# Performance work log

Hardware: AMD Instinct MI355X
Metric: run time of the kernel (lower is better)

## Reference

```python
import jax, jax.numpy as jnp
import numpy as np

N = 300000   # total atoms
E = 600000   # directed edges
G = 8192     # molecules in batch
D = 6        # node_feat_dim
H = 128      # hidden_dim
OUT = 256    # embedding_dim
L = 4        # num GIN layers


def setup_inputs() -> dict:
    key = jax.random.key(0)
    ks = jax.random.split(key, 12)
    s_in = 1.0 / np.sqrt(D)
    s_h = 1.0 / np.sqrt(H)
    return {
        "x": jax.random.normal(ks[0], (N, D), jnp.float32),
        "edge_index": jax.random.randint(ks[1], (2, E), 0, N, dtype=jnp.int32),
        "batch": jnp.sort(jax.random.randint(ks[2], (N,), 0, G, dtype=jnp.int32)),
        "W_enc": jax.random.normal(ks[3], (D, H), jnp.float32) * s_in,
        "b_enc": jnp.zeros((H,), jnp.float32),
        "W1": jax.random.normal(ks[4], (L, H, H), jnp.float32) * s_h,
        "b1": jnp.zeros((L, H), jnp.float32),
        "W2": jax.random.normal(ks[5], (L, H, H), jnp.float32) * s_h,
        "b2": jnp.zeros((L, H), jnp.float32),
        "W_out": jax.random.normal(ks[6], (H, OUT), jnp.float32) * s_h,
        "b_out": jnp.zeros((OUT,), jnp.float32),
    }


def reference(x, edge_index, batch, W_enc, b_enc, W1, b1, W2, b2, W_out, b_out):
    n = x.shape[0]
    src, dst = edge_index[0], edge_index[1]
    # node encoder
    h = x @ W_enc + b_enc                                   # [N, H]
    # stacked GINConv: out = mlp((1+eps)*x + sum_neighbors), eps = 0
    for l in range(L):
        agg = jax.ops.segment_sum(h[src], dst, num_segments=n)  # gather + scatter-add
        z = h + agg
        z = jax.nn.relu(z @ W1[l] + b1[l]) @ W2[l] + b2[l]      # GIN MLP
        h = jax.nn.relu(z)                                       # outer F.relu
    # global mean pool over graphs
    sums = jax.ops.segment_sum(h, batch, num_segments=G)        # [G, H]
    counts = jax.ops.segment_sum(jnp.ones((n, 1), h.dtype), batch, num_segments=G)
    pooled = sums / jnp.maximum(counts, 1.0)
    return pooled @ W_out + b_out                                # [G, OUT]
```

## Files before the change

kernel.cpp:

```cpp
#include <hip/hip_runtime.h>

#define HD 128

typedef unsigned short ushort_t;
typedef __attribute__((ext_vector_type(8))) unsigned short us8;
typedef __attribute__((ext_vector_type(8))) short s8b;
typedef __attribute__((ext_vector_type(16))) float f32x16;

__device__ __forceinline__ float b2f(unsigned short u) {
    union { unsigned int i; float f; } v; v.i = ((unsigned int)u) << 16; return v.f;
}
__device__ __forceinline__ unsigned short f2b(float f) {
    union { float f; unsigned int i; } v; v.f = f;
    unsigned int u = v.i;
    return (unsigned short)((u + 0x7fffu + ((u >> 16) & 1u)) >> 16);
}
__device__ __forceinline__ unsigned int pk2(float a, float b) {
    return (unsigned int)f2b(a) | ((unsigned int)f2b(b) << 16);
}

__device__ __forceinline__ void load8f(const float* p, float* o) {
    float4 a = *reinterpret_cast<const float4*>(p);
    float4 b = *reinterpret_cast<const float4*>(p + 4);
    o[0]=a.x;o[1]=a.y;o[2]=a.z;o[3]=a.w;o[4]=b.x;o[5]=b.y;o[6]=b.z;o[7]=b.w;
}
__device__ __forceinline__ void store8b(ushort_t* p, const float* s) {
    us8 v;
#pragma unroll
    for (int j = 0; j < 8; ++j) v[j] = f2b(s[j]);
    *reinterpret_cast<us8*>(p) = v;
}

__device__ __forceinline__ void store1(float* p, float v) { *p = v; }
__device__ __forceinline__ void store1(ushort_t* p, float v) { *p = f2b(v); }

__device__ __forceinline__ int lowerb(const int* __restrict__ a, int n, int v) {
    int lo = 0, hi = n;
    while (lo < hi) { int m = (lo + hi) >> 1; if (a[m] < v) lo = m + 1; else hi = m; }
    return lo;
}

__global__ void hist_kernel(const int* __restrict__ dst, int* __restrict__ deg, int e) {
    int i = blockIdx.x * blockDim.x + threadIdx.x;
    if (i < e) atomicAdd(&deg[dst[i]], 1);
}

#define SCAN_NT 256
#define SCAN_BPT 8
#define SCAN_CHUNK (SCAN_NT * SCAN_BPT)

__global__ __launch_bounds__(SCAN_NT) void scan_a(const int* __restrict__ deg,
                                                  int* __restrict__ bsum, int n) {
    int tid = threadIdx.x;
    int base = blockIdx.x * SCAN_CHUNK + tid * SCAN_BPT;
    int sum = 0;
    if (base + SCAN_BPT <= n) {
        int4 v0 = *reinterpret_cast<const int4*>(deg + base);
        int4 v1 = *reinterpret_cast<const int4*>(deg + base + 4);
        sum = v0.x + v0.y + v0.z + v0.w + v1.x + v1.y + v1.z + v1.w;
    } else {
        for (int j = 0; j < SCAN_BPT; ++j) { int i = base + j; if (i < n) sum += deg[i]; }
    }
    __shared__ int sd[SCAN_NT];
    sd[tid] = sum; __syncthreads();
    for (int off = SCAN_NT / 2; off > 0; off >>= 1) {
        if (tid < off) sd[tid] += sd[tid + off];
        __syncthreads();
    }
    if (tid == 0) bsum[blockIdx.x] = sd[0];
}

__global__ __launch_bounds__(1024) void scan_b(int* __restrict__ bsum, int nb) {
    __shared__ int ps[1024];
    int tid = threadIdx.x;
    int v = (tid < nb) ? bsum[tid] : 0;
    ps[tid] = v; __syncthreads();
    for (int off = 1; off < 1024; off <<= 1) {
        int t = (tid >= off) ? ps[tid - off] : 0;
        __syncthreads();
        ps[tid] += t;
        __syncthreads();
    }
    if (tid < nb) bsum[tid] = ps[tid] - v;
}

__global__ __launch_bounds__(SCAN_NT) void scan_c(const int* __restrict__ deg,
                                                  const int* __restrict__ bsum,
                                                  int* __restrict__ rowptr,
                                                  int* __restrict__ cursor,
                                                  int n, int etot) {
    int tid = threadIdx.x;
    int base = blockIdx.x * SCAN_CHUNK + tid * SCAN_BPT;
    int vals[SCAN_BPT];
    if (base + SCAN_BPT <= n) {
        int4 v0 = *reinterpret_cast<const int4*>(deg + base);
        int4 v1 = *reinterpret_cast<const int4*>(deg + base + 4);
        vals[0]=v0.x; vals[1]=v0.y; vals[2]=v0.z; vals[3]=v0.w;
        vals[4]=v1.x; vals[5]=v1.y; vals[6]=v1.z; vals[7]=v1.w;
    } else {
        for (int j = 0; j < SCAN_BPT; ++j) { int i = base + j; vals[j] = (i < n) ? deg[i] : 0; }
    }
    int sum = 0;
#pragma unroll
    for (int j = 0; j < SCAN_BPT; ++j) sum += vals[j];
    __shared__ int ps[SCAN_NT];
    ps[tid] = sum; __syncthreads();
    for (int off = 1; off < SCAN_NT; off <<= 1) {
        int t = (tid >= off) ? ps[tid - off] : 0;
        __syncthreads();
        ps[tid] += t;
        __syncthreads();
    }
    int run = bsum[blockIdx.x] + ps[tid] - sum;
#pragma unroll
    for (int j = 0; j < SCAN_BPT; ++j) {
        int i = base + j;
        if (i < n) { rowptr[i] = run; cursor[i] = run; run += vals[j]; }
    }
    if (blockIdx.x == 0 && tid == 0) rowptr[n] = etot;
}

__global__ void fill_kernel(const int* __restrict__ src, const int* __restrict__ dst,
                            int* __restrict__ cursor, int* __restrict__ col, int e) {
    int i = blockIdx.x * blockDim.x + threadIdx.x;
    if (i < e) { int slot = atomicAdd(&cursor[dst[i]], 1); col[slot] = src[i]; }
}

__global__ void pack_kernel(const float* __restrict__ W, ushort_t* __restrict__ Wp,
                            int nmat, int ld, int mat_stride, int col_off) {
    int idx = blockIdx.x * blockDim.x + threadIdx.x;
    if (idx >= nmat * 2048) return;
    int lane = idx & 63;
    int ks = (idx >> 6) & 7;
    int j = (idx >> 9) & 3;
    int mat = idx >> 11;
    const float* Wm = W + (size_t)mat * mat_stride;
    int k0 = ks * 16 + (lane >> 5) * 8;
    int n = mat * col_off + j * 32 + (lane & 31);
    us8 o;
#pragma unroll
    for (int e = 0; e < 8; ++e) o[e] = f2b(Wm[(size_t)(k0 + e) * ld + n]);
    *reinterpret_cast<us8*>(Wp + (size_t)idx * 8) = o;
}

__global__ void xagg_kernel(const float* __restrict__ x, const int* __restrict__ rowptr,
                            const int* __restrict__ col, float* __restrict__ xa, int n) {
    int node = blockIdx.x * blockDim.x + threadIdx.x;
    if (node >= n) return;
    const float2* xr = reinterpret_cast<const float2*>(x + (size_t)node * 6);
    float2 a0 = xr[0], a1 = xr[1], a2 = xr[2];
    int lo = rowptr[node], hi = rowptr[node + 1];
    for (int i = lo; i < hi; ++i) {
        const float2* xs = reinterpret_cast<const float2*>(x + (size_t)col[i] * 6);
        float2 s0 = xs[0], s1 = xs[1], s2 = xs[2];
        a0.x += s0.x; a0.y += s0.y; a1.x += s1.x; a1.y += s1.y; a2.x += s2.x; a2.y += s2.y;
    }
    float cnt = (float)(1 + hi - lo);
    float4 o0; o0.x = a0.x; o0.y = a0.y; o0.z = a1.x; o0.w = a1.y;
    float4 o1; o1.x = a2.x; o1.y = a2.y; o1.z = cnt; o1.w = 0.f;
    reinterpret_cast<float4*>(xa + (size_t)node * 8)[0] = o0;
    reinterpret_cast<float4*>(xa + (size_t)node * 8)[1] = o1;
}

__global__ void enc2_kernel(const float* __restrict__ xa, const float* __restrict__ W,
                            const float* __restrict__ b, ushort_t* __restrict__ z, int n) {
    int t = blockIdx.x * blockDim.x + threadIdx.x;
    int q = t >> 4, g = t & 15;
    int node0 = q * 4;
    if (node0 >= n) return;
    float w[6][8];
#pragma unroll
    for (int d = 0; d < 6; ++d) load8f(W + d * HD + g * 8, w[d]);
    float bias[8];
    load8f(b + g * 8, bias);
#pragma unroll
    for (int u = 0; u < 4; ++u) {
        int node = node0 + u;
        if (node >= n) break;
        float4 a0 = reinterpret_cast<const float4*>(xa + (size_t)node * 8)[0];
        float4 a1 = reinterpret_cast<const float4*>(xa + (size_t)node * 8)[1];
        float xv[6] = {a0.x, a0.y, a0.z, a0.w, a1.x, a1.y};
        float cnt = a1.z;
        float acc[8];
#pragma unroll
        for (int j = 0; j < 8; ++j) acc[j] = cnt * bias[j];
#pragma unroll
        for (int d = 0; d < 6; ++d)
#pragma unroll
            for (int j = 0; j < 8; ++j) acc[j] += xv[d] * w[d][j];
        store8b(z + (size_t)node * HD + g * 8, acc);
    }
}

__device__ __forceinline__ void gemm1_repack(const s8b* __restrict__ sW, const s8b* bz,
                                             const float* __restrict__ b1,
                                             int lane, int h, s8b* a2) {
#pragma unroll
    for (int j = 0; j < 4; ++j) {
        f32x16 c;
#pragma unroll
        for (int i = 0; i < 16; ++i) c[i] = 0.f;
#pragma unroll
        for (int ks = 0; ks < 8; ++ks)
            c = __builtin_amdgcn_mfma_f32_32x32x16_bf16(sW[(j * 8 + ks) * 64 + lane], bz[ks], c, 0, 0, 0);
        {
            float4 bv0 = *reinterpret_cast<const float4*>(b1 + j * 32 + 0  + 4 * h);
            float4 bv1 = *reinterpret_cast<const float4*>(b1 + j * 32 + 8  + 4 * h);
            unsigned int w00 = pk2(fmaxf(c[0] + bv0.x, 0.f), fmaxf(c[1] + bv0.y, 0.f));
            unsigned int w01 = pk2(fmaxf(c[2] + bv0.z, 0.f), fmaxf(c[3] + bv0.w, 0.f));
            unsigned int w10 = pk2(fmaxf(c[4] + bv1.x, 0.f), fmaxf(c[5] + bv1.y, 0.f));
            unsigned int w11 = pk2(fmaxf(c[6] + bv1.z, 0.f), fmaxf(c[7] + bv1.w, 0.f));
            unsigned int p00 = (unsigned int)__shfl_xor((int)w00, 32);
            unsigned int p01 = (unsigned int)__shfl_xor((int)w01, 32);
            unsigned int p10 = (unsigned int)__shfl_xor((int)w10, 32);
            unsigned int p11 = (unsigned int)__shfl_xor((int)w11, 32);
            union { unsigned int u[4]; s8b v; } t;
            t.u[0] = h ? p10 : w00;
            t.u[1] = h ? p11 : w01;
            t.u[2] = h ? w10 : p00;
            t.u[3] = h ? w11 : p01;
            a2[2 * j] = t.v;
        }
        {
            float4 bv2 = *reinterpret_cast<const float4*>(b1 + j * 32 + 16 + 4 * h);
            float4 bv3 = *reinterpret_cast<const float4*>(b1 + j * 32 + 24 + 4 * h);
            unsigned int w20 = pk2(fmaxf(c[8]  + bv2.x, 0.f), fmaxf(c[9]  + bv2.y, 0.f));
            unsigned int w21 = pk2(fmaxf(c[10] + bv2.z, 0.f), fmaxf(c[11] + bv2.w, 0.f));
            unsigned int w30 = pk2(fmaxf(c[12] + bv3.x, 0.f), fmaxf(c[13] + bv3.y, 0.f));
            unsigned int w31 = pk2(fmaxf(c[14] + bv3.z, 0.f), fmaxf(c[15] + bv3.w, 0.f));
            unsigned int p20 = (unsigned int)__shfl_xor((int)w20, 32);
            unsigned int p21 = (unsigned int)__shfl_xor((int)w21, 32);
            unsigned int p30 = (unsigned int)__shfl_xor((int)w30, 32);
            unsigned int p31 = (unsigned int)__shfl_xor((int)w31, 32);
            union { unsigned int u[4]; s8b v; } t;
            t.u[0] = h ? p30 : w20;
            t.u[1] = h ? p31 : w21;
            t.u[2] = h ? w30 : p20;
            t.u[3] = h ? w31 : p21;
            a2[2 * j + 1] = t.v;
        }
    }
}

__device__ __forceinline__ void gemm2_store(const s8b* __restrict__ sW, const s8b* a2,
                                            const float* __restrict__ b2,
                                            int lane, int h, int row0,
                                            ushort_t* __restrict__ out) {
    const int r32 = lane & 31;
#pragma unroll
    for (int j = 0; j < 4; ++j) {
        f32x16 c;
#pragma unroll
        for (int i = 0; i < 16; ++i) c[i] = 0.f;
#pragma unroll
        for (int ks = 0; ks < 8; ++ks)
            c = __builtin_amdgcn_mfma_f32_32x32x16_bf16(a2[ks], sW[(j * 8 + ks) * 64 + lane], c, 0, 0, 0);
        const int ccol = j * 32 + r32;
        const float bv = b2[ccol];
        const int rbase = row0 + 4 * h;
#pragma unroll
        for (int reg = 0; reg < 16; ++reg) {
            int row = rbase + (reg & 3) + 8 * (reg >> 2);
            out[(size_t)row * HD + ccol] = f2b(fmaxf(c[reg] + bv, 0.f));
        }
    }
}

__global__ __launch_bounds__(1024, 4) void mlp_fused(
    ushort_t* __restrict__ z,
    const ushort_t* __restrict__ Wp1, const ushort_t* __restrict__ Wp2,
    const float* __restrict__ b1, const float* __restrict__ b2)
{
    __shared__ s8b sW1[2048];
    __shared__ s8b sW2[2048];

    const int tid = threadIdx.x;
    for (int i = tid; i < 2048; i += 1024) {
        sW1[i] = reinterpret_cast<const s8b*>(Wp1)[i];
        sW2[i] = reinterpret_cast<const s8b*>(Wp2)[i];
    }
    __syncthreads();

    const int lane = tid & 63;
    const int r32  = lane & 31;
    const int h    = lane >> 5;
    const int row0 = blockIdx.x * 512 + (tid >> 6) * 32;
    const int arow = row0 + r32;
    const int koff = h * 8;

    s8b bz[8];
#pragma unroll
    for (int ks = 0; ks < 8; ++ks)
        bz[ks] = *reinterpret_cast<const s8b*>(z + (size_t)arow * HD + ks * 16 + koff);

    s8b a2[8];
    gemm1_repack(sW1, bz, b1, lane, h, a2);
    gemm2_store(sW2, a2, b2, lane, h, row0, z);
}

__global__ __launch_bounds__(1024, 4) void gin_layer(
    const ushort_t* __restrict__ hin, const int* __restrict__ rowptr,
    const int* __restrict__ col,
    const ushort_t* __restrict__ Wp1, const ushort_t* __restrict__ Wp2,
    const float* __restrict__ b1, const float* __restrict__ b2,
    ushort_t* __restrict__ hout, int n)
{
    __shared__ s8b sW1[2048];
    __shared__ s8b sW2[2048];

    const int tid = threadIdx.x;
    for (int i = tid; i < 2048; i += 1024) {
        sW1[i] = reinterpret_cast<const s8b*>(Wp1)[i];
        sW2[i] = reinterpret_cast<const s8b*>(Wp2)[i];
    }
    __syncthreads();

    const int lane = tid & 63;
    const int r32  = lane & 31;
    const int h    = lane >> 5;
    const int row0 = blockIdx.x * 512 + (tid >> 6) * 32;
    const int arow = row0 + r32;
    const int koff = h * 8;

    const bool valid = (arow < n);
    const int lo = valid ? rowptr[arow] : 0;
    const int hi = valid ? rowptr[arow + 1] : 0;
    const ushort_t* hbase = hin + (size_t)arow * HD + koff;

    s8b bz[8];

    {
        float facc[4][8];
        if (valid) {
#pragma unroll
            for (int q = 0; q < 4; ++q) {
                us8 v = *reinterpret_cast<const us8*>(hbase + q * 16);
#pragma unroll
                for (int e = 0; e < 8; ++e) facc[q][e] = b2f(v[e]);
            }
            for (int i = lo; i < hi; ++i) {
                const ushort_t* hs = hin + (size_t)col[i] * HD + koff;
#pragma unroll
                for (int q = 0; q < 4; ++q) {
                    us8 v = *reinterpret_cast<const us8*>(hs + q * 16);
#pragma unroll
                    for (int e = 0; e < 8; ++e) facc[q][e] += b2f(v[e]);
                }
            }
        } else {
#pragma unroll
            for (int q = 0; q < 4; ++q)
#pragma unroll
                for (int e = 0; e < 8; ++e) facc[q][e] = 0.f;
        }
#pragma unroll
        for (int q = 0; q < 4; ++q)
#pragma unroll
            for (int e = 0; e < 8; ++e) bz[q][e] = (short)f2b(facc[q][e]);
    }

    {
        float facc[4][8];
        if (valid) {
#pragma unroll
            for (int q = 0; q < 4; ++q) {
                us8 v = *reinterpret_cast<const us8*>(hbase + 64 + q * 16);
#pragma unroll
                for (int e = 0; e < 8; ++e) facc[q][e] = b2f(v[e]);
            }
            for (int i = lo; i < hi; ++i) {
                const ushort_t* hs = hin + (size_t)col[i] * HD + koff + 64;
#pragma unroll
                for (int q = 0; q < 4; ++q) {
                    us8 v = *reinterpret_cast<const us8*>(hs + q * 16);
#pragma unroll
                    for (int e = 0; e < 8; ++e) facc[q][e] += b2f(v[e]);
                }
            }
        } else {
#pragma unroll
            for (int q = 0; q < 4; ++q)
#pragma unroll
                for (int e = 0; e < 8; ++e) facc[q][e] = 0.f;
        }
#pragma unroll
        for (int q = 0; q < 4; ++q)
#pragma unroll
            for (int e = 0; e < 8; ++e) bz[4 + q][e] = (short)f2b(facc[q][e]);
    }

    s8b a2[8];
    gemm1_repack(sW1, bz, b1, lane, h, a2);
    gemm2_store(sW2, a2, b2, lane, h, row0, hout);
}

template<typename TO, bool RELU>
__global__ __launch_bounds__(256) void gemm_mfma(
    const ushort_t* __restrict__ A, const ushort_t* __restrict__ Wp,
    const float* __restrict__ bias, TO* __restrict__ out, int ldo)
{
    __shared__ s8b sW[2048];
    const int tid = threadIdx.x;
    for (int i = tid; i < 2048; i += 256)
        sW[i] = reinterpret_cast<const s8b*>(Wp)[i];
    __syncthreads();

    const int lane = tid & 63;
    const int row0 = blockIdx.x * 128 + (tid >> 6) * 32;
    const int arow = row0 + (lane & 31);
    const int koff = (lane >> 5) * 8;

    s8b a[8];
#pragma unroll
    for (int ks = 0; ks < 8; ++ks)
        a[ks] = *reinterpret_cast<const s8b*>(A + (size_t)arow * HD + ks * 16 + koff);

#pragma unroll
    for (int j = 0; j < 4; ++j) {
        f32x16 acc;
#pragma unroll
        for (int i = 0; i < 16; ++i) acc[i] = 0.f;
#pragma unroll
        for (int ks = 0; ks < 8; ++ks)
            acc = __builtin_amdgcn_mfma_f32_32x32x16_bf16(a[ks], sW[(j * 8 + ks) * 64 + lane], acc, 0, 0, 0);
        const int col = j * 32 + (lane & 31);
        const float bv = bias[col];
        const int rbase = row0 + 4 * (lane >> 5);
#pragma unroll
        for (int reg = 0; reg < 16; ++reg) {
            int row = rbase + (reg & 3) + 8 * (reg >> 2);
            float v = acc[reg] + bv;
            if (RELU) v = fmaxf(v, 0.f);
            store1(out + (size_t)row * ldo + col, v);
        }
    }
}

__global__ __launch_bounds__(128) void pool_kernel(const ushort_t* __restrict__ h,
                                                   const int* __restrict__ batch,
                                                   ushort_t* __restrict__ pooled, int n) {
    int g = blockIdx.x;
    int c = threadIdx.x;
    int start = lowerb(batch, n, g);
    int end = lowerb(batch, n, g + 1);
    float s = 0.f;
    for (int i = start; i < end; ++i) s += b2f(h[(size_t)i * HD + c]);
    int cnt = end - start; if (cnt < 1) cnt = 1;
    pooled[(size_t)g * HD + c] = f2b(s / (float)cnt);
}

extern "C" void kernel_launch(void* const* d_in, const int* in_sizes, int n_in,
                              void* d_out, int out_size, void* d_ws, size_t ws_size,
                              hipStream_t stream) {
    const float* x      = (const float*)d_in[0];
    const int*   edge   = (const int*)d_in[1];
    const int*   batch  = (const int*)d_in[2];
    const float* W_enc  = (const float*)d_in[3];
    const float* b_enc  = (const float*)d_in[4];
    const float* W1     = (const float*)d_in[5];
    const float* b1     = (const float*)d_in[6];
    const float* W2     = (const float*)d_in[7];
    const float* b2     = (const float*)d_in[8];
    const float* W_out  = (const float*)d_in[9];
    const float* b_out  = (const float*)d_in[10];

    const int N = in_sizes[0] / 6;
    const int E = in_sizes[1] / 2;
    const int G = out_size / 256;
    const int L = in_sizes[5] / (HD * HD);
    const int Npad = ((N + 511) / 512) * 512;

    const int* srcv = edge;
    const int* dstv = edge + E;

    size_t off = 0;
    auto alloc = [&](size_t bytes) -> char* {
        char* p = (char*)d_ws + off;
        off += (bytes + 255) & ~(size_t)255;
        return p;
    };
    ushort_t* bufA   = (ushort_t*)alloc((size_t)Npad * HD * 2);
    ushort_t* bufB   = (ushort_t*)alloc((size_t)Npad * HD * 2);
    ushort_t* pooled = (ushort_t*)alloc((size_t)G * HD * 2);
    ushort_t* Wp1    = (ushort_t*)alloc((size_t)L * 16384 * 2);
    ushort_t* Wp2    = (ushort_t*)alloc((size_t)L * 16384 * 2);
    ushort_t* WpO    = (ushort_t*)alloc((size_t)2 * 16384 * 2);
    float* xaggb = (float*)alloc((size_t)N * 8 * 4);
    int* rowptr = (int*)alloc((size_t)(N + 1) * 4);
    int* cursor = (int*)alloc((size_t)N * 4);
    int* colidx = (int*)alloc((size_t)E * 4);
    int* deg    = (int*)alloc((size_t)N * 4);
    int* bsum   = (int*)alloc((size_t)1024 * 4);
    (void)ws_size;

    const int nb = (N + SCAN_CHUNK - 1) / SCAN_CHUNK;
    hipMemsetAsync(deg, 0, (size_t)N * 4, stream);
    hist_kernel<<<(E + 255) / 256, 256, 0, stream>>>(dstv, deg, E);
    scan_a<<<nb, SCAN_NT, 0, stream>>>(deg, bsum, N);
    scan_b<<<1, 1024, 0, stream>>>(bsum, nb);
    scan_c<<<nb, SCAN_NT, 0, stream>>>(deg, bsum, rowptr, cursor, N, E);
    fill_kernel<<<(E + 255) / 256, 256, 0, stream>>>(srcv, dstv, cursor, colidx, E);

    pack_kernel<<<(L * 2048 + 255) / 256, 256, 0, stream>>>(W1, Wp1, L, HD, HD * HD, 0);
    pack_kernel<<<(L * 2048 + 255) / 256, 256, 0, stream>>>(W2, Wp2, L, HD, HD * HD, 0);
    pack_kernel<<<(2 * 2048 + 255) / 256, 256, 0, stream>>>(W_out, WpO, 2, 256, 0, 128);

    xagg_kernel<<<(N + 255) / 256, 256, 0, stream>>>(x, rowptr, colidx, xaggb, N);
    {
        int threads = ((N + 3) / 4) * 16;
        enc2_kernel<<<(threads + 255) / 256, 256, 0, stream>>>(xaggb, W_enc, b_enc, bufA, N);
    }
    const int nblk = Npad / 512;
    mlp_fused<<<nblk, 1024, 0, stream>>>(bufA, Wp1, Wp2, b1, b2);

    ushort_t* cur = bufA;
    ushort_t* oth = bufB;
    for (int l = 1; l < L; ++l) {
        gin_layer<<<nblk, 1024, 0, stream>>>(
            cur, rowptr, colidx,
            Wp1 + (size_t)l * 16384, Wp2 + (size_t)l * 16384,
            b1 + (size_t)l * HD, b2 + (size_t)l * HD, oth, N);
        ushort_t* t = cur; cur = oth; oth = t;
    }

    pool_kernel<<<G, 128, 0, stream>>>(cur, batch, pooled, N);

    float* outp = (float*)d_out;
    gemm_mfma<float, false><<<G / 128, 256, 0, stream>>>(pooled, WpO, b_out, outp, 256);
    gemm_mfma<float, false><<<G / 128, 256, 0, stream>>>(pooled, WpO + 16384, b_out + 128, outp + 128, 256);
}
```

Measured before the change: 463.4 us.

## Use persistent blocks with atomic work-stealing over 32-row tiles in GIN kernels

The fused MLP and GIN layer kernels now launch a fixed grid of 512 blocks instead of one block per 512 rows. Each wavefront repeatedly grabs a 32-row tile from a global atomic counter until all tiles are done. This spreads the uneven per-row gather cost across waves and loads the shared weights once per persistent block rather than once per tile group. In exchange it adds one atomic per tile and a memset for the counters, and the grid size is now fixed.

```diff
diff --git a/kernel.cpp b/kernel.cpp
--- a/kernel.cpp
+++ b/kernel.cpp
@@ -269,7 +269,8 @@
 __global__ __launch_bounds__(1024, 4) void mlp_fused(
     ushort_t* __restrict__ z,
     const ushort_t* __restrict__ Wp1, const ushort_t* __restrict__ Wp2,
-    const float* __restrict__ b1, const float* __restrict__ b2)
+    const float* __restrict__ b1, const float* __restrict__ b2,
+    int ntiles, int* __restrict__ counter)
 {
     __shared__ s8b sW1[2048];
     __shared__ s8b sW2[2048];
@@ -284,18 +285,25 @@
     const int lane = tid & 63;
     const int r32  = lane & 31;
     const int h    = lane >> 5;
-    const int row0 = blockIdx.x * 512 + (tid >> 6) * 32;
-    const int arow = row0 + r32;
     const int koff = h * 8;
 
-    s8b bz[8];
-#pragma unroll
-    for (int ks = 0; ks < 8; ++ks)
-        bz[ks] = *reinterpret_cast<const s8b*>(z + (size_t)arow * HD + ks * 16 + koff);
-
-    s8b a2[8];
-    gemm1_repack(sW1, bz, b1, lane, h, a2);
-    gemm2_store(sW2, a2, b2, lane, h, row0, z);
+    while (true) {
+        int t = 0;
+        if (lane == 0) t = atomicAdd(counter, 1);
+        t = __shfl(t, 0);
+        if (t >= ntiles) break;
+        const int row0 = t * 32;
+        const int arow = row0 + r32;
+
+        s8b bz[8];
+#pragma unroll
+        for (int ks = 0; ks < 8; ++ks)
+            bz[ks] = *reinterpret_cast<const s8b*>(z + (size_t)arow * HD + ks * 16 + koff);
+
+        s8b a2[8];
+        gemm1_repack(sW1, bz, b1, lane, h, a2);
+        gemm2_store(sW2, a2, b2, lane, h, row0, z);
+    }
 }
 
 __global__ __launch_bounds__(1024, 4) void gin_layer(
@@ -303,7 +311,7 @@
     const int* __restrict__ col,
     const ushort_t* __restrict__ Wp1, const ushort_t* __restrict__ Wp2,
     const float* __restrict__ b1, const float* __restrict__ b2,
-    ushort_t* __restrict__ hout, int n)
+    ushort_t* __restrict__ hout, int n, int ntiles, int* __restrict__ counter)
 {
     __shared__ s8b sW1[2048];
     __shared__ s8b sW2[2048];
@@ -318,80 +326,87 @@
     const int lane = tid & 63;
     const int r32  = lane & 31;
     const int h    = lane >> 5;
-    const int row0 = blockIdx.x * 512 + (tid >> 6) * 32;
-    const int arow = row0 + r32;
     const int koff = h * 8;
 
-    const bool valid = (arow < n);
-    const int lo = valid ? rowptr[arow] : 0;
-    const int hi = valid ? rowptr[arow + 1] : 0;
-    const ushort_t* hbase = hin + (size_t)arow * HD + koff;
-
-    s8b bz[8];
-
-    {
-        float facc[4][8];
-        if (valid) {
-#pragma unroll
-            for (int q = 0; q < 4; ++q) {
-                us8 v = *reinterpret_cast<const us8*>(hbase + q * 16);
-#pragma unroll
-                for (int e = 0; e < 8; ++e) facc[q][e] = b2f(v[e]);
+    while (true) {
+        int t = 0;
+        if (lane == 0) t = atomicAdd(counter, 1);
+        t = __shfl(t, 0);
+        if (t >= ntiles) break;
+        const int row0 = t * 32;
+        const int arow = row0 + r32;
+
+        const bool valid = (arow < n);
+        const int lo = valid ? rowptr[arow] : 0;
+        const int hi = valid ? rowptr[arow + 1] : 0;
+        const ushort_t* hbase = hin + (size_t)arow * HD + koff;
+
+        s8b bz[8];
+
+        {
+            float facc[4][8];
+            if (valid) {
+#pragma unroll
+                for (int q = 0; q < 4; ++q) {
+                    us8 v = *reinterpret_cast<const us8*>(hbase + q * 16);
+#pragma unroll
+                    for (int e = 0; e < 8; ++e) facc[q][e] = b2f(v[e]);
+                }
+                for (int i = lo; i < hi; ++i) {
+                    const ushort_t* hs = hin + (size_t)col[i] * HD + koff;
+#pragma unroll
+                    for (int q = 0; q < 4; ++q) {
+                        us8 v = *reinterpret_cast<const us8*>(hs + q * 16);
+#pragma unroll
+                        for (int e = 0; e < 8; ++e) facc[q][e] += b2f(v[e]);
+                    }
+                }
+            } else {
+#pragma unroll
+                for (int q = 0; q < 4; ++q)
+#pragma unroll
+                    for (int e = 0; e < 8; ++e) facc[q][e] = 0.f;
             }
-            for (int i = lo; i < hi; ++i) {
-                const ushort_t* hs = hin + (size_t)col[i] * HD + koff;
+#pragma unroll
+            for (int q = 0; q < 4; ++q)
+#pragma unroll
+                for (int e = 0; e < 8; ++e) bz[q][e] = (short)f2b(facc[q][e]);
+        }
+
+        {
+            float facc[4][8];
+            if (valid) {
 #pragma unroll
                 for (int q = 0; q < 4; ++q) {
-                    us8 v = *reinterpret_cast<const us8*>(hs + q * 16);
-#pragma unroll
-                    for (int e = 0; e < 8; ++e) facc[q][e] += b2f(v[e]);
+                    us8 v = *reinterpret_cast<const us8*>(hbase + 64 + q * 16);
+#pragma unroll
+                    for (int e = 0; e < 8; ++e) facc[q][e] = b2f(v[e]);
                 }
+                for (int i = lo; i < hi; ++i) {
+                    const ushort_t* hs = hin + (size_t)col[i] * HD + koff + 64;
+#pragma unroll
+                    for (int q = 0; q < 4; ++q) {
+                        us8 v = *reinterpret_cast<const us8*>(hs + q * 16);
+#pragma unroll
+                        for (int e = 0; e < 8; ++e) facc[q][e] += b2f(v[e]);
+                    }
+                }
+            } else {
+#pragma unroll
+                for (int q = 0; q < 4; ++q)
+#pragma unroll
+                    for (int e = 0; e < 8; ++e) facc[q][e] = 0.f;
             }
-        } else {
 #pragma unroll
             for (int q = 0; q < 4; ++q)
 #pragma unroll
-                for (int e = 0; e < 8; ++e) facc[q][e] = 0.f;
+                for (int e = 0; e < 8; ++e) bz[4 + q][e] = (short)f2b(facc[q][e]);
         }
-#pragma unroll
-        for (int q = 0; q < 4; ++q)
-#pragma unroll
-            for (int e = 0; e < 8; ++e) bz[q][e] = (short)f2b(facc[q][e]);
-    }
-
-    {
-        float facc[4][8];
-        if (valid) {
-#pragma unroll
-            for (int q = 0; q < 4; ++q) {
-                us8 v = *reinterpret_cast<const us8*>(hbase + 64 + q * 16);
-#pragma unroll
-                for (int e = 0; e < 8; ++e) facc[q][e] = b2f(v[e]);
-            }
-            for (int i = lo; i < hi; ++i) {
-                const ushort_t* hs = hin + (size_t)col[i] * HD + koff + 64;
-#pragma unroll
-                for (int q = 0; q < 4; ++q) {
-                    us8 v = *reinterpret_cast<const us8*>(hs + q * 16);
-#pragma unroll
-                    for (int e = 0; e < 8; ++e) facc[q][e] += b2f(v[e]);
-                }
-            }
-        } else {
-#pragma unroll
-            for (int q = 0; q < 4; ++q)
-#pragma unroll
-                for (int e = 0; e < 8; ++e) facc[q][e] = 0.f;
-        }
-#pragma unroll
-        for (int q = 0; q < 4; ++q)
-#pragma unroll
-            for (int e = 0; e < 8; ++e) bz[4 + q][e] = (short)f2b(facc[q][e]);
-    }
-
-    s8b a2[8];
-    gemm1_repack(sW1, bz, b1, lane, h, a2);
-    gemm2_store(sW2, a2, b2, lane, h, row0, hout);
+
+        s8b a2[8];
+        gemm1_repack(sW1, bz, b1, lane, h, a2);
+        gemm2_store(sW2, a2, b2, lane, h, row0, hout);
+    }
 }
 
 template<typename TO, bool RELU>
@@ -469,6 +484,7 @@
     const int G = out_size / 256;
     const int L = in_sizes[5] / (HD * HD);
     const int Npad = ((N + 511) / 512) * 512;
+    const int ntiles = (N + 31) / 32;
 
     const int* srcv = edge;
     const int* dstv = edge + E;
@@ -491,7 +507,10 @@
     int* colidx = (int*)alloc((size_t)E * 4);
     int* deg    = (int*)alloc((size_t)N * 4);
     int* bsum   = (int*)alloc((size_t)1024 * 4);
+    int* counters = (int*)alloc((size_t)16 * 4);
     (void)ws_size;
+
+    hipMemsetAsync(counters, 0, 16 * 4, stream);
 
     const int nb = (N + SCAN_CHUNK - 1) / SCAN_CHUNK;
     hipMemsetAsync(deg, 0, (size_t)N * 4, stream);
@@ -510,16 +529,16 @@
         int threads = ((N + 3) / 4) * 16;
         enc2_kernel<<<(threads + 255) / 256, 256, 0, stream>>>(xaggb, W_enc, b_enc, bufA, N);
     }
-    const int nblk = Npad / 512;
-    mlp_fused<<<nblk, 1024, 0, stream>>>(bufA, Wp1, Wp2, b1, b2);
+    const int PBLK = 512;
+    mlp_fused<<<PBLK, 1024, 0, stream>>>(bufA, Wp1, Wp2, b1, b2, ntiles, counters + 0);
 
     ushort_t* cur = bufA;
     ushort_t* oth = bufB;
     for (int l = 1; l < L; ++l) {
-        gin_layer<<<nblk, 1024, 0, stream>>>(
+        gin_layer<<<PBLK, 1024, 0, stream>>>(
             cur, rowptr, colidx,
             Wp1 + (size_t)l * 16384, Wp2 + (size_t)l * 16384,
-            b1 + (size_t)l * HD, b2 + (size_t)l * HD, oth, N);
+            b1 + (size_t)l * HD, b2 + (size_t)l * HD, oth, N, ntiles, counters + l);
         ushort_t* t = cur; cur = oth; oth = t;
     }
 
```

Result: slower. 1.061 ms (+128.9%).
